# Optimization experiments

Measured on AMD Instinct MI355X. Metric: run time of the kernel, lower is better.

Reference implementation:

```python
import jax, jax.numpy as jnp
import numpy as np

N, D, F_NUM = 262144, 128, 64
TEMPERATURE = 0.5
EPS = 1e-8  # torch F.cosine_similarity eps


def setup_inputs() -> dict:
    key = jax.random.key(0)
    k1, k2 = jax.random.split(key)
    embeddings = jax.random.normal(k1, (N, D), dtype=jnp.float32)
    families = jax.random.randint(k2, (N,), 0, F_NUM, dtype=jnp.int32)
    return {"embeddings": embeddings, "families": families}


def reference(embeddings, families):
    T = TEMPERATURE
    n = embeddings.shape[0]
    # Per-family prototype means (segment mean). All F_NUM families are
    # present w.h.p.; guard counts with max(.,1) to avoid div-by-zero.
    ones = jnp.ones((n,), dtype=embeddings.dtype)
    counts = jax.ops.segment_sum(ones, families, num_segments=F_NUM)
    sums = jax.ops.segment_sum(embeddings, families, num_segments=F_NUM)
    protos = sums / jnp.maximum(counts, 1.0)[:, None]  # [F, D]

    # Cosine similarity matrix [N, F], matching torch eps semantics:
    # x.y / max(||x|| * ||y||, eps)
    dots = embeddings @ protos.T                              # [N, F]
    e_norm = jnp.linalg.norm(embeddings, axis=1)              # [N]
    p_norm = jnp.linalg.norm(protos, axis=1)                  # [F]
    sim = dots / jnp.maximum(e_norm[:, None] * p_norm[None, :], EPS)

    pos = jnp.take_along_axis(sim, families[:, None].astype(jnp.int32), axis=1)[:, 0]  # [N]
    # Source quirk: logits already divided by T, then divided by T again
    # inside logsumexp -> effective sim / T^2. The concatenated logits
    # contain pos + all other prototypes = all F prototypes exactly once.
    lse = jax.nn.logsumexp(sim / (T * T), axis=1)             # [N]
    per_sample = -pos / T + lse                               # [N]
    loss = jnp.sum(per_sample) / n
    return loss[None]  # torch returns shape (1,)
```

## Files before the change

kernel.cpp:

```cpp
#include <hip/hip_runtime.h>
#include <math.h>


#define D_DIM 128
#define F_NUM 64
#define ROWS_A 512

typedef __attribute__((ext_vector_type(8))) short short8;
typedef __attribute__((ext_vector_type(4))) float f32x4;

static __device__ __forceinline__ unsigned short f2bf(float x) {
  union { float f; unsigned u; } v; v.f = x;
  unsigned r = v.u + 0x7FFFu + ((v.u >> 16) & 1u);
  return (unsigned short)(r >> 16);
}

__global__ __launch_bounds__(256, 2) void pass_a(
    const float* __restrict__ emb, const int* __restrict__ fam,
    float* __restrict__ psum)
{
  int t = threadIdx.x, w = t >> 6, lane = t & 63;
  int m16 = lane & 15, q = lane >> 4;
  int dimBase = w * 32;

  f32x4 acc[4][2] = {};
  int rb0 = blockIdx.x * ROWS_A;

  #pragma unroll 2
  for (int s = 0; s < ROWS_A / 32; ++s) {
    int rb = rb0 + s * 32;
    const int* fp = fam + rb + q * 8;
    int fj[8];
    #pragma unroll
    for (int j = 0; j < 8; ++j) fj[j] = fp[j];

    const float* eb = emb + (size_t)(rb + q * 8) * D_DIM + dimBase + m16;
    float x0[8], x1[8];
    #pragma unroll
    for (int j = 0; j < 8; ++j) {
      x0[j] = eb[j * D_DIM];
      x1[j] = eb[j * D_DIM + 16];
    }

    short8 af[4];
    #pragma unroll
    for (int ft = 0; ft < 4; ++ft)
      #pragma unroll
      for (int j = 0; j < 8; ++j)
        af[ft][j] = (fj[j] == ft * 16 + m16) ? (short)0x3F80 : (short)0;

    short8 h0, l0, h1, l1;
    #pragma unroll
    for (int j = 0; j < 8; ++j) {
      unsigned b0 = __float_as_uint(x0[j]);
      h0[j] = (short)(b0 >> 16);
      l0[j] = (short)f2bf(x0[j] - __uint_as_float(b0 & 0xFFFF0000u));
      unsigned b1 = __float_as_uint(x1[j]);
      h1[j] = (short)(b1 >> 16);
      l1[j] = (short)f2bf(x1[j] - __uint_as_float(b1 & 0xFFFF0000u));
    }

    #pragma unroll
    for (int ft = 0; ft < 4; ++ft) {
      acc[ft][0] = __builtin_amdgcn_mfma_f32_16x16x32_bf16(af[ft], h0, acc[ft][0], 0, 0, 0);
      acc[ft][0] = __builtin_amdgcn_mfma_f32_16x16x32_bf16(af[ft], l0, acc[ft][0], 0, 0, 0);
      acc[ft][1] = __builtin_amdgcn_mfma_f32_16x16x32_bf16(af[ft], h1, acc[ft][1], 0, 0, 0);
      acc[ft][1] = __builtin_amdgcn_mfma_f32_16x16x32_bf16(af[ft], l1, acc[ft][1], 0, 0, 0);
    }
  }

  float* outp = psum + (size_t)blockIdx.x * (F_NUM * D_DIM) + dimBase + m16;
  #pragma unroll
  for (int ft = 0; ft < 4; ++ft)
    #pragma unroll
    for (int i = 0; i < 4; ++i) {
      int f = ft * 16 + q * 4 + i;
      outp[(size_t)f * D_DIM]      = acc[ft][0][i];
      outp[(size_t)f * D_DIM + 16] = acc[ft][1][i];
    }
}

__global__ __launch_bounds__(256) void pass_b(
    const float* __restrict__ psum, unsigned short* __restrict__ protoB,
    float* __restrict__ out, int nPart)
{
  __shared__ float4 sh[256];
  int t = threadIdx.x, f = blockIdx.x;
  if (f == 0 && t == 0) out[0] = 0.f;
  int d4 = t & 31, pg = t >> 5;
  const float4* p4 = (const float4*)psum;
  float4 s = make_float4(0.f, 0.f, 0.f, 0.f);
  int per = nPart >> 3;
  #pragma unroll 8
  for (int i = 0; i < per; ++i) {
    float4 a = p4[(size_t)(pg + 8 * i) * (F_NUM * D_DIM / 4) + f * 32 + d4];
    s.x += a.x; s.y += a.y; s.z += a.z; s.w += a.w;
  }
  sh[t] = s;
  __syncthreads();
  if (t < 32) {
    float4 rsum = sh[t];
    #pragma unroll
    for (int g = 1; g < 8; ++g) {
      float4 a = sh[g * 32 + t];
      rsum.x += a.x; rsum.y += a.y; rsum.z += a.z; rsum.w += a.w;
    }
    float n2 = rsum.x * rsum.x + rsum.y * rsum.y +
               rsum.z * rsum.z + rsum.w * rsum.w;
    n2 += __shfl_xor(n2, 1);  n2 += __shfl_xor(n2, 2);  n2 += __shfl_xor(n2, 4);
    n2 += __shfl_xor(n2, 8);  n2 += __shfl_xor(n2, 16);
    float inv = rsqrtf(fmaxf(n2, 1e-24f));
    ushort4 u;
    u.x = f2bf(rsum.x * inv); u.y = f2bf(rsum.y * inv);
    u.z = f2bf(rsum.z * inv); u.w = f2bf(rsum.w * inv);
    ((ushort4*)protoB)[f * 32 + t] = u;
  }
}

__global__ __launch_bounds__(256) void pass_c(
    const float* __restrict__ emb, const int* __restrict__ fam,
    const unsigned short* __restrict__ protoB,
    float* __restrict__ out, float invN)
{
  __shared__ float sWp[4];
  int t = threadIdx.x, w = t >> 6, lane = t & 63;
  int m16 = lane & 15, q = lane >> 4;
  int S0 = blockIdx.x * 128 + w * 32;

  const float4* E4 = (const float4*)emb;
  const short8* P8 = (const short8*)protoB;

  size_t e0 = (size_t)(S0 + m16) * 32 + q * 2;
  size_t e1 = e0 + 16 * 32;
  int pb = m16 * 16 + q;

  f32x4 acc[2][4] = {};
  float s2a = 0.f, s2b = 0.f;

  #pragma unroll
  for (int ks = 0; ks < 4; ++ks) {
    short8 a0 = P8[pb + ks * 4];
    short8 a1 = P8[pb + 256 + ks * 4];
    short8 a2 = P8[pb + 512 + ks * 4];
    short8 a3 = P8[pb + 768 + ks * 4];

    float4 va = E4[e0 + ks * 8], vb = E4[e0 + ks * 8 + 1];
    s2a += va.x * va.x + va.y * va.y + va.z * va.z + va.w * va.w +
           vb.x * vb.x + vb.y * vb.y + vb.z * vb.z + vb.w * vb.w;
    short8 b0;
    b0[0] = (short)f2bf(va.x); b0[1] = (short)f2bf(va.y);
    b0[2] = (short)f2bf(va.z); b0[3] = (short)f2bf(va.w);
    b0[4] = (short)f2bf(vb.x); b0[5] = (short)f2bf(vb.y);
    b0[6] = (short)f2bf(vb.z); b0[7] = (short)f2bf(vb.w);
    acc[0][0] = __builtin_amdgcn_mfma_f32_16x16x32_bf16(a0, b0, acc[0][0], 0, 0, 0);
    acc[0][1] = __builtin_amdgcn_mfma_f32_16x16x32_bf16(a1, b0, acc[0][1], 0, 0, 0);
    acc[0][2] = __builtin_amdgcn_mfma_f32_16x16x32_bf16(a2, b0, acc[0][2], 0, 0, 0);
    acc[0][3] = __builtin_amdgcn_mfma_f32_16x16x32_bf16(a3, b0, acc[0][3], 0, 0, 0);

    float4 vc = E4[e1 + ks * 8], vd = E4[e1 + ks * 8 + 1];
    s2b += vc.x * vc.x + vc.y * vc.y + vc.z * vc.z + vc.w * vc.w +
           vd.x * vd.x + vd.y * vd.y + vd.z * vd.z + vd.w * vd.w;
    short8 b1;
    b1[0] = (short)f2bf(vc.x); b1[1] = (short)f2bf(vc.y);
    b1[2] = (short)f2bf(vc.z); b1[3] = (short)f2bf(vc.w);
    b1[4] = (short)f2bf(vd.x); b1[5] = (short)f2bf(vd.y);
    b1[6] = (short)f2bf(vd.z); b1[7] = (short)f2bf(vd.w);
    acc[1][0] = __builtin_amdgcn_mfma_f32_16x16x32_bf16(a0, b1, acc[1][0], 0, 0, 0);
    acc[1][1] = __builtin_amdgcn_mfma_f32_16x16x32_bf16(a1, b1, acc[1][1], 0, 0, 0);
    acc[1][2] = __builtin_amdgcn_mfma_f32_16x16x32_bf16(a2, b1, acc[1][2], 0, 0, 0);
    acc[1][3] = __builtin_amdgcn_mfma_f32_16x16x32_bf16(a3, b1, acc[1][3], 0, 0, 0);
  }

  s2a += __shfl_xor(s2a, 16); s2a += __shfl_xor(s2a, 32);
  s2b += __shfl_xor(s2b, 16); s2b += __shfl_xor(s2b, 32);
  float rn0 = rsqrtf(fmaxf(s2a, 1e-20f));
  float rn1 = rsqrtf(fmaxf(s2b, 1e-20f));
  int fr0 = fam[S0 + m16], fr1 = fam[S0 + 16 + m16];

  float wp = 0.f;
  {
    int fh = fr0 >> 4, fq = (fr0 >> 2) & 3, fl = fr0 & 3;
    float es = 0.f, ps = 0.f;
    #pragma unroll
    for (int ft = 0; ft < 4; ++ft)
      #pragma unroll
      for (int i = 0; i < 4; ++i) {
        float sim = acc[0][ft][i] * rn0;
        es += __expf(4.f * sim - 4.f);
        ps += (fq == q && fh == ft && fl == i) ? sim : 0.f;
      }
    es += __shfl_xor(es, 16); es += __shfl_xor(es, 32);
    ps += __shfl_xor(ps, 16); ps += __shfl_xor(ps, 32);
    if (q == 0) wp += 4.f + __logf(es) - 2.f * ps;
  }
  {
    int fh = fr1 >> 4, fq = (fr1 >> 2) & 3, fl = fr1 & 3;
    float es = 0.f, ps = 0.f;
    #pragma unroll
    for (int ft = 0; ft < 4; ++ft)
      #pragma unroll
      for (int i = 0; i < 4; ++i) {
        float sim = acc[1][ft][i] * rn1;
        es += __expf(4.f * sim - 4.f);
        ps += (fq == q && fh == ft && fl == i) ? sim : 0.f;
      }
    es += __shfl_xor(es, 16); es += __shfl_xor(es, 32);
    ps += __shfl_xor(ps, 16); ps += __shfl_xor(ps, 32);
    if (q == 0) wp += 4.f + __logf(es) - 2.f * ps;
  }

  wp += __shfl_xor(wp, 1);  wp += __shfl_xor(wp, 2);  wp += __shfl_xor(wp, 4);
  wp += __shfl_xor(wp, 8);  wp += __shfl_xor(wp, 16); wp += __shfl_xor(wp, 32);
  if (lane == 0) sWp[w] = wp;
  __syncthreads();
  if (t == 0)
    unsafeAtomicAdd(out, (sWp[0] + sWp[1] + sWp[2] + sWp[3]) * invN);
}

extern "C" void kernel_launch(void* const* d_in, const int* in_sizes, int n_in,
                              void* d_out, int out_size, void* d_ws, size_t ws_size,
                              hipStream_t stream) {
  const float* emb = (const float*)d_in[0];
  const int* fam = (const int*)d_in[1];
  int N = in_sizes[0] / D_DIM;
  int blocksA = N / ROWS_A;
  int blocksC = N / 128;

  float* ws = (float*)d_ws;
  float* psum = ws;
  unsigned short* protoB = (unsigned short*)(ws + (size_t)blocksA * (F_NUM * D_DIM));

  pass_a<<<blocksA, 256, 0, stream>>>(emb, fam, psum);
  pass_b<<<F_NUM, 256, 0, stream>>>(psum, protoB, (float*)d_out, blocksA);
  pass_c<<<blocksC, 256, 0, stream>>>(emb, fam, protoB, (float*)d_out,
                                      1.0f / (float)N);
}
```

Measured before the change: 246.5 us.

## Fuse segment-sum and prototype normalize kernels via global atomic counter barrier

Merges pass_a and pass_b into one kernel. Every block writes its partial sums and increments a global counter. The first 64 blocks then spin until all blocks have arrived, and each reduces one family's prototype. This removes a kernel launch and its gap, but adds a memset node and spin-waiting blocks that could in principle deadlock if the waiting blocks occupy slots needed by blocks that have not yet been scheduled. With 512 blocks at 2 per CU, the whole grid should be resident at once.

```diff
diff --git a/kernel.cpp b/kernel.cpp
--- a/kernel.cpp
+++ b/kernel.cpp
@@ -15,105 +15,120 @@
   return (unsigned short)(r >> 16);
 }
 
-__global__ __launch_bounds__(256, 2) void pass_a(
+__global__ __launch_bounds__(256, 2) void pass_ab(
     const float* __restrict__ emb, const int* __restrict__ fam,
-    float* __restrict__ psum)
+    float* __restrict__ psum, unsigned short* __restrict__ protoB,
+    float* __restrict__ out, unsigned int* __restrict__ cnt, int nBlk)
 {
-  int t = threadIdx.x, w = t >> 6, lane = t & 63;
+  __shared__ float4 sh[256];
+  int t = threadIdx.x, blk = blockIdx.x;
+  int w = t >> 6, lane = t & 63;
   int m16 = lane & 15, q = lane >> 4;
-  int dimBase = w * 32;
-
-  f32x4 acc[4][2] = {};
-  int rb0 = blockIdx.x * ROWS_A;
-
-  #pragma unroll 2
-  for (int s = 0; s < ROWS_A / 32; ++s) {
-    int rb = rb0 + s * 32;
-    const int* fp = fam + rb + q * 8;
-    int fj[8];
-    #pragma unroll
-    for (int j = 0; j < 8; ++j) fj[j] = fp[j];
-
-    const float* eb = emb + (size_t)(rb + q * 8) * D_DIM + dimBase + m16;
-    float x0[8], x1[8];
-    #pragma unroll
-    for (int j = 0; j < 8; ++j) {
-      x0[j] = eb[j * D_DIM];
-      x1[j] = eb[j * D_DIM + 16];
+
+  if (blk == 0 && t == 0) out[0] = 0.f;
+
+  {
+    int dimBase = w * 32;
+    f32x4 acc[4][2] = {};
+    int rb0 = blk * ROWS_A;
+
+    #pragma unroll 2
+    for (int s = 0; s < ROWS_A / 32; ++s) {
+      int rb = rb0 + s * 32;
+      const int* fp = fam + rb + q * 8;
+      int fj[8];
+      #pragma unroll
+      for (int j = 0; j < 8; ++j) fj[j] = fp[j];
+
+      const float* eb = emb + (size_t)(rb + q * 8) * D_DIM + dimBase + m16;
+      float x0[8], x1[8];
+      #pragma unroll
+      for (int j = 0; j < 8; ++j) {
+        x0[j] = eb[j * D_DIM];
+        x1[j] = eb[j * D_DIM + 16];
+      }
+
+      short8 af[4];
+      #pragma unroll
+      for (int ft = 0; ft < 4; ++ft)
+        #pragma unroll
+        for (int j = 0; j < 8; ++j)
+          af[ft][j] = (fj[j] == ft * 16 + m16) ? (short)0x3F80 : (short)0;
+
+      short8 h0, l0, h1, l1;
+      #pragma unroll
+      for (int j = 0; j < 8; ++j) {
+        unsigned b0 = __float_as_uint(x0[j]);
+        h0[j] = (short)(b0 >> 16);
+        l0[j] = (short)f2bf(x0[j] - __uint_as_float(b0 & 0xFFFF0000u));
+        unsigned b1 = __float_as_uint(x1[j]);
+        h1[j] = (short)(b1 >> 16);
+        l1[j] = (short)f2bf(x1[j] - __uint_as_float(b1 & 0xFFFF0000u));
+      }
+
+      #pragma unroll
+      for (int ft = 0; ft < 4; ++ft) {
+        acc[ft][0] = __builtin_amdgcn_mfma_f32_16x16x32_bf16(af[ft], h0, acc[ft][0], 0, 0, 0);
+        acc[ft][0] = __builtin_amdgcn_mfma_f32_16x16x32_bf16(af[ft], l0, acc[ft][0], 0, 0, 0);
+        acc[ft][1] = __builtin_amdgcn_mfma_f32_16x16x32_bf16(af[ft], h1, acc[ft][1], 0, 0, 0);
+        acc[ft][1] = __builtin_amdgcn_mfma_f32_16x16x32_bf16(af[ft], l1, acc[ft][1], 0, 0, 0);
+      }
     }
 
-    short8 af[4];
+    float* outp = psum + (size_t)blk * (F_NUM * D_DIM) + dimBase + m16;
     #pragma unroll
     for (int ft = 0; ft < 4; ++ft)
       #pragma unroll
-      for (int j = 0; j < 8; ++j)
-        af[ft][j] = (fj[j] == ft * 16 + m16) ? (short)0x3F80 : (short)0;
-
-    short8 h0, l0, h1, l1;
-    #pragma unroll
-    for (int j = 0; j < 8; ++j) {
-      unsigned b0 = __float_as_uint(x0[j]);
-      h0[j] = (short)(b0 >> 16);
-      l0[j] = (short)f2bf(x0[j] - __uint_as_float(b0 & 0xFFFF0000u));
-      unsigned b1 = __float_as_uint(x1[j]);
-      h1[j] = (short)(b1 >> 16);
-      l1[j] = (short)f2bf(x1[j] - __uint_as_float(b1 & 0xFFFF0000u));
+      for (int i = 0; i < 4; ++i) {
+        int f = ft * 16 + q * 4 + i;
+        outp[(size_t)f * D_DIM]      = acc[ft][0][i];
+        outp[(size_t)f * D_DIM + 16] = acc[ft][1][i];
+      }
+  }
+
+  __threadfence();
+  __syncthreads();
+  if (t == 0)
+    __hip_atomic_fetch_add(cnt, 1u, __ATOMIC_ACQ_REL, __HIP_MEMORY_SCOPE_AGENT);
+  if (blk >= F_NUM) return;
+
+  if (t == 0) {
+    while (__hip_atomic_load(cnt, __ATOMIC_ACQUIRE, __HIP_MEMORY_SCOPE_AGENT)
+           < (unsigned)nBlk)
+      __builtin_amdgcn_s_sleep(8);
+  }
+  __syncthreads();
+  __threadfence();
+
+  {
+    int f = blk, d4 = t & 31, pg = t >> 5;
+    const float4* p4 = (const float4*)psum;
+    float4 s = make_float4(0.f, 0.f, 0.f, 0.f);
+    int per = nBlk >> 3;
+    #pragma unroll 8
+    for (int i = 0; i < per; ++i) {
+      float4 a = p4[(size_t)(pg + 8 * i) * (F_NUM * D_DIM / 4) + f * 32 + d4];
+      s.x += a.x; s.y += a.y; s.z += a.z; s.w += a.w;
     }
-
-    #pragma unroll
-    for (int ft = 0; ft < 4; ++ft) {
-      acc[ft][0] = __builtin_amdgcn_mfma_f32_16x16x32_bf16(af[ft], h0, acc[ft][0], 0, 0, 0);
-      acc[ft][0] = __builtin_amdgcn_mfma_f32_16x16x32_bf16(af[ft], l0, acc[ft][0], 0, 0, 0);
-      acc[ft][1] = __builtin_amdgcn_mfma_f32_16x16x32_bf16(af[ft], h1, acc[ft][1], 0, 0, 0);
-      acc[ft][1] = __builtin_amdgcn_mfma_f32_16x16x32_bf16(af[ft], l1, acc[ft][1], 0, 0, 0);
+    sh[t] = s;
+    __syncthreads();
+    if (t < 32) {
+      float4 rsum = sh[t];
+      #pragma unroll
+      for (int g = 1; g < 8; ++g) {
+        float4 a = sh[g * 32 + t];
+        rsum.x += a.x; rsum.y += a.y; rsum.z += a.z; rsum.w += a.w;
+      }
+      float n2 = rsum.x * rsum.x + rsum.y * rsum.y +
+                 rsum.z * rsum.z + rsum.w * rsum.w;
+      n2 += __shfl_xor(n2, 1);  n2 += __shfl_xor(n2, 2);  n2 += __shfl_xor(n2, 4);
+      n2 += __shfl_xor(n2, 8);  n2 += __shfl_xor(n2, 16);
+      float inv = rsqrtf(fmaxf(n2, 1e-24f));
+      ushort4 u;
+      u.x = f2bf(rsum.x * inv); u.y = f2bf(rsum.y * inv);
+      u.z = f2bf(rsum.z * inv); u.w = f2bf(rsum.w * inv);
+      ((ushort4*)protoB)[f * 32 + t] = u;
     }
-  }
-
-  float* outp = psum + (size_t)blockIdx.x * (F_NUM * D_DIM) + dimBase + m16;
-  #pragma unroll
-  for (int ft = 0; ft < 4; ++ft)
-    #pragma unroll
-    for (int i = 0; i < 4; ++i) {
-      int f = ft * 16 + q * 4 + i;
-      outp[(size_t)f * D_DIM]      = acc[ft][0][i];
-      outp[(size_t)f * D_DIM + 16] = acc[ft][1][i];
-    }
-}
-
-__global__ __launch_bounds__(256) void pass_b(
-    const float* __restrict__ psum, unsigned short* __restrict__ protoB,
-    float* __restrict__ out, int nPart)
-{
-  __shared__ float4 sh[256];
-  int t = threadIdx.x, f = blockIdx.x;
-  if (f == 0 && t == 0) out[0] = 0.f;
-  int d4 = t & 31, pg = t >> 5;
-  const float4* p4 = (const float4*)psum;
-  float4 s = make_float4(0.f, 0.f, 0.f, 0.f);
-  int per = nPart >> 3;
-  #pragma unroll 8
-  for (int i = 0; i < per; ++i) {
-    float4 a = p4[(size_t)(pg + 8 * i) * (F_NUM * D_DIM / 4) + f * 32 + d4];
-    s.x += a.x; s.y += a.y; s.z += a.z; s.w += a.w;
-  }
-  sh[t] = s;
-  __syncthreads();
-  if (t < 32) {
-    float4 rsum = sh[t];
-    #pragma unroll
-    for (int g = 1; g < 8; ++g) {
-      float4 a = sh[g * 32 + t];
-      rsum.x += a.x; rsum.y += a.y; rsum.z += a.z; rsum.w += a.w;
-    }
-    float n2 = rsum.x * rsum.x + rsum.y * rsum.y +
-               rsum.z * rsum.z + rsum.w * rsum.w;
-    n2 += __shfl_xor(n2, 1);  n2 += __shfl_xor(n2, 2);  n2 += __shfl_xor(n2, 4);
-    n2 += __shfl_xor(n2, 8);  n2 += __shfl_xor(n2, 16);
-    float inv = rsqrtf(fmaxf(n2, 1e-24f));
-    ushort4 u;
-    u.x = f2bf(rsum.x * inv); u.y = f2bf(rsum.y * inv);
-    u.z = f2bf(rsum.z * inv); u.w = f2bf(rsum.w * inv);
-    ((ushort4*)protoB)[f * 32 + t] = u;
   }
 }
 
@@ -228,10 +243,13 @@
 
   float* ws = (float*)d_ws;
   float* psum = ws;
-  unsigned short* protoB = (unsigned short*)(ws + (size_t)blocksA * (F_NUM * D_DIM));
-
-  pass_a<<<blocksA, 256, 0, stream>>>(emb, fam, psum);
-  pass_b<<<F_NUM, 256, 0, stream>>>(psum, protoB, (float*)d_out, blocksA);
+  size_t off = (size_t)blocksA * (F_NUM * D_DIM);
+  unsigned short* protoB = (unsigned short*)(ws + off); off += (F_NUM * D_DIM) / 2;
+  unsigned int* cnt = (unsigned int*)(ws + off);
+
+  (void)hipMemsetAsync(cnt, 0, sizeof(unsigned int), stream);
+  pass_ab<<<blocksA, 256, 0, stream>>>(emb, fam, psum, protoB,
+                                       (float*)d_out, cnt, blocksA);
   pass_c<<<blocksC, 256, 0, stream>>>(emb, fam, protoB, (float*)d_out,
                                       1.0f / (float)N);
 }
```

New measurement: 347.5 us. +41.0%, slower.
